# Kernel tuning notes

Measured on AMD Instinct MI355X. Metric: run time of the kernel, lower is better.

Reference implementation:

```python
import jax, jax.numpy as jnp
import numpy as np
import math

G_GRAPHS = 32   # graphs per batch
NPG = 2048      # nodes per graph
DEG = 8         # avg degree
IN_DIM = 128
HID = 128

def _lin(k, fi, fo):
    return jax.random.normal(k, (fi, fo), jnp.float32) / np.sqrt(fi).astype(np.float32)

def setup_inputs():
    key = jax.random.key(0)
    ks = jax.random.split(key, 32)
    Nt = G_GRAPHS * NPG
    Epg = NPG * DEG
    E = G_GRAPHS * Epg
    x = jax.random.normal(ks[0], (Nt, IN_DIM), jnp.float32)
    src = jax.random.randint(ks[1], (E,), 0, NPG)
    dst = jax.random.randint(ks[2], (E,), 0, NPG)
    off = (jnp.arange(E) // Epg) * NPG  # keep edges within their graph block
    edge_index = jnp.stack([src + off, dst + off]).astype(jnp.int32)
    batch = (jnp.arange(Nt) // NPG).astype(jnp.int32)
    p = {}
    dims = [(IN_DIM, HID), (HID, HID), (HID, HID), (HID, HID)]
    for i, (fi, fo) in enumerate(dims, 1):
        p['Wl%d' % i] = _lin(ks[3 * i], fi, fo)
        p['bl%d' % i] = jnp.zeros((fo,), jnp.float32)
        p['Wr%d' % i] = _lin(ks[3 * i + 1], fi, fo)
    for j in (1, 2):  # SAGPooling score GNN (GraphConv hidden->1)
        p['Prel%d' % j] = _lin(ks[15 + 2 * j], HID, 1)
        p['prb%d' % j] = jnp.zeros((1,), jnp.float32)
        p['Proot%d' % j] = _lin(ks[16 + 2 * j], HID, 1)
    p['W5'] = _lin(ks[24], HID, 64); p['b5'] = jnp.zeros((64,), jnp.float32)
    p['W6'] = _lin(ks[25], 64, 2);  p['b6'] = jnp.zeros((2,), jnp.float32)
    return dict(x=x, edge_index=edge_index, batch=batch, npg=NPG, **p)

def reference(x, edge_index, batch, npg,
              Wl1, bl1, Wr1, Wl2, bl2, Wr2, Wl3, bl3, Wr3, Wl4, bl4, Wr4,
              Prel1, prb1, Proot1, Prel2, prb2, Proot2, W5, b5, W6, b6):
    src, dst = edge_index[0], edge_index[1]
    Nt = x.shape[0]
    Gn = Nt // npg

    def sage(h, em, Wl, bl, Wr):
        # SAGEConv (mean aggr): lin_l(mean_j x_j) + lin_r(x_root)
        s = jax.ops.segment_sum(h[src] * em[:, None], dst, num_segments=Nt)
        c = jax.ops.segment_sum(em, dst, num_segments=Nt)
        return (s / jnp.maximum(c, 1.0)[:, None]) @ Wl + bl + h @ Wr

    def pool(h, em, nm, k, Prel, prb, Proot):
        # SAGPooling: score = GraphConv(h) (add aggr), top-k per graph, x *= tanh(score)
        s = jax.ops.segment_sum(h[src] * em[:, None], dst, num_segments=Nt)
        score = (s @ Prel + h @ Proot + prb)[:, 0]
        smr = jnp.where(nm > 0, score, -1e30).reshape(Gn, npg)
        _, idx = jax.lax.top_k(smr, k)
        newm = jnp.zeros((Gn, npg), h.dtype).at[jnp.arange(Gn)[:, None], idx].set(1.0).reshape(-1)
        h = h * jnp.tanh(score)[:, None] * newm[:, None]
        em = em * newm[src] * newm[dst]  # filter_adj: keep edges with both ends kept
        return h, em, newm

    em = jnp.ones(src.shape, x.dtype)
    nm = jnp.ones((Nt,), x.dtype)
    h = jax.nn.relu(sage(x, em, Wl1, bl1, Wr1))
    h = jax.nn.relu(sage(h, em, Wl2, bl2, Wr2))
    k1 = math.ceil(0.5 * npg)
    h, em, nm = pool(h, em, nm, k1, Prel1, prb1, Proot1)
    h = jax.nn.relu(sage(h, em, Wl3, bl3, Wr3)) * nm[:, None]
    h = jax.nn.relu(sage(h, em, Wl4, bl4, Wr4)) * nm[:, None]
    k2 = math.ceil(0.5 * k1)
    h, em, nm = pool(h, em, nm, k2, Prel2, prb2, Proot2)
    # global mean pool over surviving nodes
    sums = jax.ops.segment_sum(h, batch, num_segments=Gn)
    cnt = jax.ops.segment_sum(nm, batch, num_segments=Gn)
    g = sums / jnp.maximum(cnt, 1.0)[:, None]
    g = jax.nn.relu(g @ W5 + b5)
    return jax.nn.log_softmax(g @ W6 + b6, axis=1)
```

## Files before the change

### kernel.cpp

```cpp
#include <hip/hip_runtime.h>
#include <hip/hip_bf16.h>
#include <math.h>

#define NT   65536
#define NPGC 2048
#define NG   32
#define NE   524288
#define HID  128
#define K1   1024
#define K2   512

typedef short short8 __attribute__((ext_vector_type(8)));
typedef float f32x4  __attribute__((ext_vector_type(4)));

__device__ __forceinline__ float bf2f(unsigned short u) {
    union { unsigned int i; float f; } v; v.i = ((unsigned int)u) << 16; return v.f;
}
__device__ __forceinline__ unsigned short f2bf(float f) {
    union { float f; unsigned int i; } v; v.f = f;
    unsigned int x = v.i;
    return (unsigned short)((x + 0x7fffu + ((x >> 16) & 1u)) >> 16);
}
__device__ __forceinline__ void split2(float v, unsigned short& hi, unsigned short& lo) {
    unsigned int b = __float_as_uint(v);
    hi = (unsigned short)(b >> 16);
    float rem = v - __uint_as_float(b & 0xFFFF0000u);
    lo = (unsigned short)(__float_as_uint(rem) >> 16);
}

__global__ void k_detect(const unsigned short* __restrict__ x, int* __restrict__ flag) {
    __shared__ int cnt;
    if (threadIdx.x == 0) cnt = 0;
    __syncthreads();
    int sane = 0;
#pragma unroll
    for (int j = 0; j < 16; ++j) {
        unsigned short u = x[threadIdx.x * 16 + j];
        int e = (u >> 7) & 0xFF;
        if (e > 0x60 && e < 0xA0) sane++;
    }
    atomicAdd(&cnt, sane);
    __syncthreads();
    if (threadIdx.x == 0) *flag = (cnt > 3686) ? 1 : 0;
}

struct CvtDesc { const void* src[22]; int n[22]; int off[22]; };

__global__ void k_cvt(CvtDesc d, float* __restrict__ wts, const int* __restrict__ flag) {
    int t = blockIdx.y;
    int n = d.n[t];
    bool isbf = (*flag != 0);
    const unsigned short* sb = (const unsigned short*)d.src[t];
    const float* sf = (const float*)d.src[t];
    float* o = wts + d.off[t];
    for (int i = blockIdx.x * blockDim.x + threadIdx.x; i < n; i += gridDim.x * blockDim.x)
        o[i] = isbf ? bf2f(sb[i]) : sf[i];
}

__global__ void k_packW(const float* __restrict__ wts, int4 oWl, int4 oWr,
                        unsigned short* __restrict__ Wpack,
                        int* __restrict__ rowc, int* __restrict__ fill) {
    int idx = blockIdx.x * 256 + threadIdx.x;
    if (idx < NT) { rowc[idx] = 0; fill[idx] = 0; }
    if (idx >= 4 * 8 * 8 * 64 * 8) return;
    int L    = idx >> 15;
    int rem  = idx & 32767;
    int ct   = rem >> 12;
    int rem2 = rem & 4095;
    int ks   = rem2 >> 9;
    int rem3 = rem2 & 511;
    int lane = rem3 >> 3;
    int j    = rem3 & 7;
    int k   = ks * 32 + (lane >> 4) * 8 + j;
    int col = ct * 16 + (lane & 15);
    int ol = (L == 0) ? oWl.x : (L == 1) ? oWl.y : (L == 2) ? oWl.z : oWl.w;
    int orr = (L == 0) ? oWr.x : (L == 1) ? oWr.y : (L == 2) ? oWr.z : oWr.w;
    float w = (k < 128) ? wts[ol + k * 128 + col] : wts[orr + (k - 128) * 128 + col];
    unsigned short hi = f2bf(w);
    unsigned short lo = f2bf(w - bf2f(hi));
    int base = L * 65536 + (ct * 8 + ks) * 512 + lane * 8 + j;
    Wpack[base]         = hi;
    Wpack[base + 32768] = lo;
}

__global__ void k_load_x(const void* __restrict__ x, float* __restrict__ out,
                         const int* __restrict__ flag, int n4,
                         float* __restrict__ nm, const int* __restrict__ dstE,
                         int* __restrict__ rowc) {
    int i = blockIdx.x * blockDim.x + threadIdx.x;
    if (i < NT) nm[i] = 1.0f;
    if (i < NE) atomicAdd(&rowc[dstE[i]], 1);
    if (i >= n4) return;
    if (*flag) {
        ushort4 v = ((const ushort4*)x)[i];
        float4 o;
        o.x = bf2f(v.x); o.y = bf2f(v.y); o.z = bf2f(v.z); o.w = bf2f(v.w);
        ((float4*)out)[i] = o;
    }
}

__global__ void k_scan1(const int* __restrict__ cnt, int* __restrict__ rp, int* __restrict__ bsum,
                        float* __restrict__ invc) {
    __shared__ int s[256];
    int t = threadIdx.x;
    int i = blockIdx.x * 256 + t;
    int v = cnt[i];
    invc[i] = 1.0f / fmaxf((float)v, 1.0f);
    s[t] = v;
    __syncthreads();
    for (int off = 1; off < 256; off <<= 1) {
        int a = (t >= off) ? s[t - off] : 0;
        __syncthreads();
        s[t] += a;
        __syncthreads();
    }
    rp[i] = s[t] - v;
    if (t == 255) bsum[blockIdx.x] = s[255];
}

__global__ void k_scan23(int* __restrict__ rp, const int* __restrict__ bsum) {
    __shared__ int s[256];
    int t = threadIdx.x;
    s[t] = bsum[t];
    __syncthreads();
    for (int off = 1; off < 256; off <<= 1) {
        int a = (t >= off) ? s[t - off] : 0;
        __syncthreads();
        s[t] += a;
        __syncthreads();
    }
    int boffv = s[blockIdx.x] - bsum[blockIdx.x];
    int i = blockIdx.x * 256 + t;
    rp[i] += boffv;
    if (i == 0) rp[NT] = NE;
}

__global__ void k_scatter(const int* __restrict__ src, const int* __restrict__ dst,
                          const int* __restrict__ rp, int* __restrict__ fill, int* __restrict__ col) {
    int e = blockIdx.x * blockDim.x + threadIdx.x;
    if (e < NE) {
        int d = dst[e];
        int p = rp[d] + atomicAdd(&fill[d], 1);
        col[p] = src[e];
    }
}

__global__ void k_invc(const float* __restrict__ nm, const int* __restrict__ rp,
                       const int* __restrict__ col, float* __restrict__ invc,
                       const int* __restrict__ act) {
    int n = act[blockIdx.x * 256 + threadIdx.x];
    int beg = rp[n], end = rp[n + 1];
    float c = 0.f;
    for (int e = beg; e < end; ++e) c += nm[col[e]];
    invc[n] = 1.0f / fmaxf(c, 1.0f);
}

__device__ __forceinline__ int lds_sw(int node, int k) {
    int g = k >> 3;
    int go = g ^ (node & 7);
    return node * 128 + go * 8 + (k & 7);
}

template<bool HAS_TS, bool COMPACT>
__device__ __forceinline__ void sage_body(
    const float* __restrict__ h, const float* __restrict__ ts,
    const float* __restrict__ nm, const float* __restrict__ invc,
    const int* __restrict__ rp, const int* __restrict__ col,
    const unsigned short* __restrict__ Wp,
    unsigned short* Ahi, unsigned short* Alo,
    int n0, const int* sact, int tid, f32x4 acc[2][2])
{
    int lane = tid & 63, w = tid >> 6;
    int lrow = lane & 15, quad = lane >> 4;

#pragma unroll
    for (int pass = 0; pass < 4; ++pass) {
        int node = pass * 8 + (tid >> 5);
        int f = (tid & 31) * 4;
        int gn = COMPACT ? sact[node] : n0 + node;
        float ax = 0.f, ay = 0.f, az = 0.f, aw = 0.f;
        bool active = COMPACT ? true : (nm[gn] > 0.f);
        if (active) {
            int beg = rp[gn], end = rp[gn + 1];
            for (int e0 = beg; e0 < end; e0 += 4) {
                int ecl = end - 1;
                int e1 = (e0 + 1 < end) ? e0 + 1 : ecl;
                int e2 = (e0 + 2 < end) ? e0 + 2 : ecl;
                int e3 = (e0 + 3 < end) ? e0 + 3 : ecl;
                int s0 = col[e0], s1 = col[e1], s2 = col[e2], s3 = col[e3];
                float4 v0 = *(const float4*)&h[(size_t)s0 * HID + f];
                float4 v1 = *(const float4*)&h[(size_t)s1 * HID + f];
                float4 v2 = *(const float4*)&h[(size_t)s2 * HID + f];
                float4 v3 = *(const float4*)&h[(size_t)s3 * HID + f];
                float c0 = HAS_TS ? ts[s0] : 1.0f;
                float c1 = (e0 + 1 < end) ? (HAS_TS ? ts[s1] : 1.0f) : 0.0f;
                float c2 = (e0 + 2 < end) ? (HAS_TS ? ts[s2] : 1.0f) : 0.0f;
                float c3 = (e0 + 3 < end) ? (HAS_TS ? ts[s3] : 1.0f) : 0.0f;
                ax += v0.x * c0 + v1.x * c1 + v2.x * c2 + v3.x * c3;
                ay += v0.y * c0 + v1.y * c1 + v2.y * c2 + v3.y * c3;
                az += v0.z * c0 + v1.z * c1 + v2.z * c2 + v3.z * c3;
                aw += v0.w * c0 + v1.w * c1 + v2.w * c2 + v3.w * c3;
            }
        }
        float inv = invc[gn];
        ushort4 hi4, lo4;
        split2(ax * inv, hi4.x, lo4.x);
        split2(ay * inv, hi4.y, lo4.y);
        split2(az * inv, hi4.z, lo4.z);
        split2(aw * inv, hi4.w, lo4.w);
        int a = lds_sw(node, f);
        *(ushort4*)&Ahi[a] = hi4;
        *(ushort4*)&Alo[a] = lo4;
    }
    __syncthreads();

#pragma unroll
    for (int ks = 0; ks < 4; ++ks) {
        short8 bh[2], blo[2];
#pragma unroll
        for (int c = 0; c < 2; ++c) {
            int ct = 2 * w + c;
            bh[c]  = *(const short8*)&Wp[(ct * 8 + ks) * 512 + lane * 8];
            blo[c] = *(const short8*)&Wp[32768 + (ct * 8 + ks) * 512 + lane * 8];
        }
        int kb = ks * 32 + quad * 8;
#pragma unroll
        for (int st = 0; st < 2; ++st) {
            int a = lds_sw(st * 16 + lrow, kb);
            short8 ah = *(const short8*)&Ahi[a];
            short8 al = *(const short8*)&Alo[a];
#pragma unroll
            for (int c = 0; c < 2; ++c) {
                acc[st][c] = __builtin_amdgcn_mfma_f32_16x16x32_bf16(ah, bh[c],  acc[st][c], 0, 0, 0);
                acc[st][c] = __builtin_amdgcn_mfma_f32_16x16x32_bf16(al, bh[c],  acc[st][c], 0, 0, 0);
                acc[st][c] = __builtin_amdgcn_mfma_f32_16x16x32_bf16(ah, blo[c], acc[st][c], 0, 0, 0);
            }
        }
    }
    __syncthreads();

#pragma unroll
    for (int i = 0; i < 4; ++i) {
        int idx = i * 256 + tid;
        int node = idx >> 5;
        int f = (idx & 31) * 4;
        int gn = COMPACT ? sact[node] : n0 + node;
        float4 v = *(const float4*)&h[(size_t)gn * HID + f];
        float sc = HAS_TS ? ts[gn] : 1.0f;
        ushort4 hi4, lo4;
        split2(v.x * sc, hi4.x, lo4.x);
        split2(v.y * sc, hi4.y, lo4.y);
        split2(v.z * sc, hi4.z, lo4.z);
        split2(v.w * sc, hi4.w, lo4.w);
        int a = lds_sw(node, f);
        *(ushort4*)&Ahi[a] = hi4;
        *(ushort4*)&Alo[a] = lo4;
    }
    __syncthreads();

#pragma unroll
    for (int ks = 4; ks < 8; ++ks) {
        short8 bh[2], blo[2];
#pragma unroll
        for (int c = 0; c < 2; ++c) {
            int ct = 2 * w + c;
            bh[c]  = *(const short8*)&Wp[(ct * 8 + ks) * 512 + lane * 8];
            blo[c] = *(const short8*)&Wp[32768 + (ct * 8 + ks) * 512 + lane * 8];
        }
        int kb = (ks - 4) * 32 + quad * 8;
#pragma unroll
        for (int st = 0; st < 2; ++st) {
            int a = lds_sw(st * 16 + lrow, kb);
            short8 ah = *(const short8*)&Ahi[a];
            short8 al = *(const short8*)&Alo[a];
#pragma unroll
            for (int c = 0; c < 2; ++c) {
                acc[st][c] = __builtin_amdgcn_mfma_f32_16x16x32_bf16(ah, bh[c],  acc[st][c], 0, 0, 0);
                acc[st][c] = __builtin_amdgcn_mfma_f32_16x16x32_bf16(al, bh[c],  acc[st][c], 0, 0, 0);
                acc[st][c] = __builtin_amdgcn_mfma_f32_16x16x32_bf16(ah, blo[c], acc[st][c], 0, 0, 0);
            }
        }
    }
}

template<bool COMPACT>
__device__ __forceinline__ void map_block(int b, int& graph, int& tile) {
    if (COMPACT) { graph = (b & 7) * 4 + (b >> 8); tile = (b >> 3) & 31; }
    else         { graph = (b & 7) * 4 + (b >> 9); tile = (b >> 3) & 63; }
}

template<bool HAS_TS, bool COMPACT>
__global__ void __launch_bounds__(256, 8) k_sage_plain(
    const float* __restrict__ h, const void* __restrict__ xraw, const int* __restrict__ flag,
    const float* __restrict__ ts,
    const float* __restrict__ nm, const float* __restrict__ invc,
    const int* __restrict__ rp, const int* __restrict__ col,
    const unsigned short* __restrict__ Wp, const float* __restrict__ bl,
    float* __restrict__ out, const int* __restrict__ act)
{
    __shared__ unsigned short Ahi[32 * 128];
    __shared__ unsigned short Alo[32 * 128];
    __shared__ int sact[32];
    int tid = threadIdx.x;
    int graph, tile;
    map_block<COMPACT>(blockIdx.x, graph, tile);
    int n0 = graph * NPGC + tile * 32;
    if (COMPACT) {
        if (tid < 32) sact[tid] = act[graph * K1 + tile * 32 + tid];
        __syncthreads();
    }
    int lane = tid & 63, w = tid >> 6;
    int lrow = lane & 15, quad = lane >> 4;
    f32x4 acc[2][2] = {};

    const float* hh = h;
    if (!COMPACT && xraw && *flag == 0) hh = (const float*)xraw;

    sage_body<HAS_TS, COMPACT>(hh, ts, nm, invc, rp, col, Wp, Ahi, Alo, n0, sact, tid, acc);

#pragma unroll
    for (int c = 0; c < 2; ++c) {
        int colg = (2 * w + c) * 16 + lrow;
        float bias = bl[colg];
#pragma unroll
        for (int st = 0; st < 2; ++st) {
#pragma unroll
            for (int rr = 0; rr < 4; ++rr) {
                int nl = st * 16 + quad * 4 + rr;
                int node = COMPACT ? sact[nl] : n0 + nl;
                float val = fmaxf(acc[st][c][rr] + bias, 0.f);
                if (!COMPACT) val *= nm[node];
                out[(size_t)node * HID + colg] = val;
            }
        }
    }
}

template<bool HAS_TS, bool COMPACT>
__global__ void __launch_bounds__(256, 8) k_sage_dots(
    const float* __restrict__ h, const float* __restrict__ ts,
    const float* __restrict__ nm, const float* __restrict__ invc,
    const int* __restrict__ rp, const int* __restrict__ col,
    const unsigned short* __restrict__ Wp, const float* __restrict__ bl,
    float* __restrict__ out,
    const float* __restrict__ Prel, const float* __restrict__ Proot,
    float* __restrict__ q, float* __restrict__ r, const int* __restrict__ act)
{
    __shared__ unsigned short Ahi[32 * 128];
    __shared__ unsigned short Alo[32 * 128];
    __shared__ int sact[32];
    int tid = threadIdx.x;
    int graph, tile;
    map_block<COMPACT>(blockIdx.x, graph, tile);
    int n0 = graph * NPGC + tile * 32;
    if (COMPACT) {
        if (tid < 32) sact[tid] = act[graph * K1 + tile * 32 + tid];
        __syncthreads();
    }
    int lane = tid & 63, w = tid >> 6;
    int lrow = lane & 15, quad = lane >> 4;
    f32x4 acc[2][2] = {};

    sage_body<HAS_TS, COMPACT>(h, ts, nm, invc, rp, col, Wp, Ahi, Alo, n0, sact, tid, acc);

    float qp[2][4] = {}, rp_[2][4] = {};
#pragma unroll
    for (int c = 0; c < 2; ++c) {
        int colg = (2 * w + c) * 16 + lrow;
        float bias = bl[colg];
        float pq = Prel[colg], pr = Proot[colg];
#pragma unroll
        for (int st = 0; st < 2; ++st) {
#pragma unroll
            for (int rr = 0; rr < 4; ++rr) {
                int nl = st * 16 + quad * 4 + rr;
                int node = COMPACT ? sact[nl] : n0 + nl;
                float val = fmaxf(acc[st][c][rr] + bias, 0.f);
                if (!COMPACT) val *= nm[node];
                out[(size_t)node * HID + colg] = val;
                qp[st][rr] += val * pq;
                rp_[st][rr] += val * pr;
            }
        }
    }
#pragma unroll
    for (int st = 0; st < 2; ++st)
#pragma unroll
        for (int rr = 0; rr < 4; ++rr) {
#pragma unroll
            for (int m = 1; m < 16; m <<= 1) {
                qp[st][rr]  += __shfl_xor(qp[st][rr],  m, 64);
                rp_[st][rr] += __shfl_xor(rp_[st][rr], m, 64);
            }
        }
    __syncthreads();
    float* qa = (float*)Ahi;
    if (tid < 64) qa[tid] = 0.f;
    __syncthreads();
    if (lrow == 0) {
#pragma unroll
        for (int st = 0; st < 2; ++st)
#pragma unroll
            for (int rr = 0; rr < 4; ++rr) {
                int nl = st * 16 + quad * 4 + rr;
                atomicAdd(&qa[nl], qp[st][rr]);
                atomicAdd(&qa[32 + nl], rp_[st][rr]);
            }
    }
    __syncthreads();
    if (tid < 32) {
        int node = COMPACT ? sact[tid] : n0 + tid;
        q[node] = qa[tid];
        r[node] = qa[32 + tid];
    }
}

__global__ void k_score(const float* __restrict__ q, const float* __restrict__ r,
                        const float* __restrict__ prb,
                        const int* __restrict__ rp, const int* __restrict__ col,
                        float* __restrict__ score) {
    int n = blockIdx.x * 256 + threadIdx.x;
    int beg = rp[n], end = rp[n + 1];
    float s = 0.f;
    for (int e = beg; e < end; ++e) s += q[col[e]];
    score[n] = s + r[n] + prb[0];
}

template<bool ZQ>
__global__ void __launch_bounds__(256) k_topk(const float* __restrict__ score,
                                              float* __restrict__ nm,
                                              float* __restrict__ tval, int k,
                                              int* __restrict__ act,
                                              float* __restrict__ q) {
    __shared__ unsigned int u[NPGC];
    __shared__ int hist[256];
    __shared__ int scanb[257];
    __shared__ int wtot[4];
    __shared__ int wtot2[4];
    __shared__ unsigned int s_byte;
    __shared__ int s_kk;
    int tid = threadIdx.x;
    int lane = tid & 63, wv = tid >> 6;
    int base = blockIdx.x * NPGC;

    for (int j = tid; j < NPGC; j += 256) {
        float sc = (nm[base + j] > 0.f) ? score[base + j] : -1e30f;
        unsigned int v = __float_as_uint(sc);
        v = (v & 0x80000000u) ? ~v : (v | 0x80000000u);
        u[j] = v;
    }
    hist[tid] = 0;
    if (tid == 0) scanb[256] = 0;
    __syncthreads();

    unsigned int prefix = 0;
    int kk = k;
#pragma unroll
    for (int round = 0; round < 4; ++round) {
        int shift = 24 - 8 * round;
        unsigned int pmask = (round == 0) ? 0u : (0xFFFFFFFFu << (32 - 8 * round));
        for (int j = tid; j < NPGC; j += 256) {
            unsigned int v = u[j];
            if ((v & pmask) == prefix) atomicAdd(&hist[(v >> shift) & 0xFF], 1);
        }
        __syncthreads();
        int s = hist[tid];
#pragma unroll
        for (int off = 1; off < 64; off <<= 1) {
            int t = __shfl_down(s, off, 64);
            s += (lane + off < 64) ? t : 0;
        }
        if (lane == 0) wtot[wv] = s;
        __syncthreads();
        int add = 0;
#pragma unroll
        for (int w2 = 1; w2 < 4; ++w2) add += (wv + w2 < 4) ? wtot[wv + w2] : 0;
        s += add;
        scanb[tid] = s;
        __syncthreads();
        int above = scanb[tid + 1];
        if (s >= kk && above < kk) { s_byte = (unsigned int)tid; s_kk = kk - above; }
        hist[tid] = 0;
        __syncthreads();
        prefix |= (s_byte << shift);
        kk = s_kk;
    }
    unsigned int thr = prefix;

    int j0 = tid * 8;
    int cnt = 0;
#pragma unroll
    for (int j = 0; j < 8; ++j) cnt += (u[j0 + j] == thr);
    int s = cnt;
#pragma unroll
    for (int off = 1; off < 64; off <<= 1) {
        int t = __shfl_up(s, off, 64);
        s += (lane >= off) ? t : 0;
    }
    if (lane == 63) wtot[wv] = s;
    __syncthreads();
    int add = 0;
#pragma unroll
    for (int w2 = 0; w2 < 4; ++w2) add += (w2 < wv) ? wtot[w2] : 0;
    int rank = s - cnt + add;

    unsigned int keepmask = 0u;
    int myrank = rank;
    int kcnt = 0;
#pragma unroll
    for (int j = 0; j < 8; ++j) {
        unsigned int v = u[j0 + j];
        bool kp;
        if (v > thr) kp = true;
        else if (v == thr) { kp = (myrank < kk); myrank++; }
        else kp = false;
        keepmask |= (kp ? 1u : 0u) << j;
        kcnt += kp ? 1 : 0;
    }
    int s2 = kcnt;
#pragma unroll
    for (int off = 1; off < 64; off <<= 1) {
        int t2 = __shfl_up(s2, off, 64);
        s2 += (lane >= off) ? t2 : 0;
    }
    if (lane == 63) wtot2[wv] = s2;
    __syncthreads();
    int pos = s2 - kcnt;
#pragma unroll
    for (int w2 = 0; w2 < 4; ++w2) pos += (w2 < wv) ? wtot2[w2] : 0;
    int* actg = act + blockIdx.x * k;
#pragma unroll
    for (int j = 0; j < 8; ++j) {
        bool kp = (keepmask >> j) & 1u;
        int n = base + j0 + j;
        nm[n]   = kp ? 1.0f : 0.0f;
        tval[n] = kp ? tanhf(score[n]) : 0.0f;
        if (kp)      { actg[pos++] = n; }
        else if (ZQ) { q[n] = 0.0f; }
    }
}

__global__ void k_gsum(const float* __restrict__ h, const float* __restrict__ t,
                       const int* __restrict__ act, float* __restrict__ g) {
    int b = blockIdx.x;
    int graph = b >> 2, part = b & 3;
    int f = threadIdx.x & 127, sub = threadIdx.x >> 7;
    int base = graph * K2 + part * 128 + sub * 64;
    float acc = 0.f;
#pragma unroll 4
    for (int n = 0; n < 64; ++n) {
        int gn = act[base + n];
        acc += h[(size_t)gn * HID + f] * t[gn];
    }
    atomicAdd(&g[graph * HID + f], acc);
}

__global__ void k_mlp(const float* __restrict__ g,
                      const float* __restrict__ W5,
                      const float* __restrict__ b5, const float* __restrict__ W6,
                      const float* __restrict__ b6, void* __restrict__ out,
                      const int* __restrict__ flag) {
    __shared__ float g5[64];
    __shared__ float ls[2];
    int graph = blockIdx.x, j = threadIdx.x;
    const float ic = 1.0f / (float)K2;
    float acc = b5[j];
    for (int f = 0; f < HID; ++f)
        acc += (g[graph * HID + f] * ic) * W5[f * 64 + j];
    g5[j] = fmaxf(acc, 0.f);
    __syncthreads();
    if (j < 2) {
        float l = b6[j];
        for (int t = 0; t < 64; ++t) l += g5[t] * W6[t * 2 + j];
        ls[j] = l;
    }
    __syncthreads();
    if (j == 0) {
        float a = ls[0], b = ls[1];
        float mx = fmaxf(a, b);
        float lse = mx + logf(expf(a - mx) + expf(b - mx));
        if (*flag) {
            ((unsigned short*)out)[graph * 2 + 0] = f2bf(a - lse);
            ((unsigned short*)out)[graph * 2 + 1] = f2bf(b - lse);
        } else {
            ((float*)out)[graph * 2 + 0] = a - lse;
            ((float*)out)[graph * 2 + 1] = b - lse;
        }
    }
}

extern "C" void kernel_launch(void* const* d_in, const int* in_sizes, int n_in,
                              void* d_out, int out_size, void* d_ws, size_t ws_size,
                              hipStream_t stream) {
    const void* x    = d_in[0];
    const int*  ei   = (const int*)d_in[1];
    const int*  srcE = ei;
    const int*  dstE = ei + NE;

    char* ws = (char*)d_ws;
    float* hA    = (float*)(ws + 0);
    float* hB    = (float*)(ws + 33554432);
    float* tvec  = (float*)(ws + 67108864);
    float* invc  = (float*)(ws + 67371008);
    float* q     = (float*)(ws + 100663296);
    float* r     = (float*)(ws + 100925440);
    float* score = (float*)(ws + 101187584);
    float* nm    = (float*)(ws + 101449728);
    int*   rowc  = (int*)  (ws + 101711872);
    int*   rp    = (int*)  (ws + 101974016);
    int*   bsum  = (int*)  (ws + 102236416);
    int*   fill  = (int*)  (ws + 102238464);
    int*   col   = (int*)  (ws + 102500608);
    float* g     = (float*)(ws + 104597760);
    int*   flag  = (int*)  (ws + 104615936);
    float* wts   = (float*)(ws + 104616960);
    unsigned short* Wpack = (unsigned short*)(ws + 105179136);
    int*   act1  = rowc;
    int*   act2  = fill;
    (void)in_sizes; (void)n_in; (void)out_size; (void)ws_size;

    const int O_Wl1 = 0,      O_bl1 = 16384,  O_Wr1 = 16512;
    const int O_Wl2 = 32896,  O_bl2 = 49280,  O_Wr2 = 49408;
    const int O_Wl3 = 65792,  O_bl3 = 82176,  O_Wr3 = 82304;
    const int O_Wl4 = 98688,  O_bl4 = 115072, O_Wr4 = 115200;
    const int O_Pr1 = 131584, O_pb1 = 131712, O_Po1 = 131713;
    const int O_Pr2 = 131841, O_pb2 = 131969, O_Po2 = 131970;
    const int O_W5  = 132098, O_b5  = 140290, O_W6 = 140354, O_b6 = 140482;

    CvtDesc d;
    const int srcIdx[22] = {4,5,6,7,8,9,10,11,12,13,14,15,16,17,18,19,20,21,22,23,24,25};
    const int nelems[22] = {16384,128,16384, 16384,128,16384, 16384,128,16384, 16384,128,16384,
                            128,1,128, 128,1,128, 8192,64,128,2};
    const int offs[22]   = {O_Wl1,O_bl1,O_Wr1, O_Wl2,O_bl2,O_Wr2, O_Wl3,O_bl3,O_Wr3, O_Wl4,O_bl4,O_Wr4,
                            O_Pr1,O_pb1,O_Po1, O_Pr2,O_pb2,O_Po2, O_W5,O_b5,O_W6,O_b6};
    for (int i = 0; i < 22; ++i) { d.src[i] = d_in[srcIdx[i]]; d.n[i] = nelems[i]; d.off[i] = offs[i]; }

    hipMemsetAsync(g, 0, (NG * HID + NG + 64) * 4, stream);

    k_detect <<<1, 256, 0, stream>>>((const unsigned short*)x, flag);
    k_cvt    <<<dim3(64, 22), 256, 0, stream>>>(d, wts, flag);
    k_packW  <<<512, 256, 0, stream>>>(wts, make_int4(O_Wl1, O_Wl2, O_Wl3, O_Wl4),
                                       make_int4(O_Wr1, O_Wr2, O_Wr3, O_Wr4), Wpack, rowc, fill);
    k_load_x <<<8192, 256, 0, stream>>>(x, hA, flag, NT * HID / 4, nm, dstE, rowc);

    k_scan1  <<<256, 256, 0, stream>>>(rowc, rp, bsum, invc);
    k_scan23 <<<256, 256, 0, stream>>>(rp, bsum);
    k_scatter<<<2048, 256, 0, stream>>>(srcE, dstE, rp, fill, col);

    k_sage_plain<false, false><<<2048, 256, 0, stream>>>(hA, x, flag, nullptr, nm, invc, rp, col,
                                                         Wpack + 0 * 65536, wts + O_bl1, hB, nullptr);
    k_sage_dots<false, false><<<2048, 256, 0, stream>>>(hB, nullptr, nm, invc, rp, col,
                                                        Wpack + 1 * 65536, wts + O_bl2, hA,
                                                        wts + O_Pr1, wts + O_Po1, q, r, nullptr);

    k_score<<<256, 256, 0, stream>>>(q, r, wts + O_pb1, rp, col, score);
    k_topk<true><<<32, 256, 0, stream>>>(score, nm, tvec, K1, act1, q);
    k_invc <<<NG * K1 / 256, 256, 0, stream>>>(nm, rp, col, invc, act1);

    k_sage_plain<true, true><<<1024, 256, 0, stream>>>(hA, nullptr, flag, tvec, nm, invc, rp, col,
                                                       Wpack + 2 * 65536, wts + O_bl3, hB, act1);
    k_sage_dots<true, true><<<1024, 256, 0, stream>>>(hB, nm, nm, invc, rp, col,
                                                      Wpack + 3 * 65536, wts + O_bl4, hA,
                                                      wts + O_Pr2, wts + O_Po2, q, r, act1);

    k_score<<<256, 256, 0, stream>>>(q, r, wts + O_pb2, rp, col, score);
    k_topk<false><<<32, 256, 0, stream>>>(score, nm, tvec, K2, act2, nullptr);

    k_gsum<<<NG * 4, 256, 0, stream>>>(hA, tvec, act2, g);
    k_mlp <<<32, 64, 0, stream>>>(g, wts + O_W5, wts + O_b5, wts + O_W6, wts + O_b6, d_out, flag);
}
```

Measured before the change: 369.4 us.

## Prefetch root features, double LDS buffers, widen gather, score only active nodes

The SAGE body now loads root-node features into registers before the neighbour gather. It stages them in a second pair of LDS buffers, so the two GEMM halves run as one 8-step loop with a single barrier instead of three. The gather loop is unrolled to 8 edges per iteration to keep more loads in flight. Active-node indices are read straight from global memory instead of being staged in LDS. The second score kernel runs only over the surviving active nodes. Occupancy is lowered (launch bounds 8 to 4 blocks) to fit the doubled LDS and the extra registers, trading some latency hiding for more memory-level parallelism per thread.

```diff
diff --git a/kernel.cpp b/kernel.cpp
--- a/kernel.cpp
+++ b/kernel.cpp
@@ -168,38 +168,53 @@
     const int* __restrict__ rp, const int* __restrict__ col,
     const unsigned short* __restrict__ Wp,
     unsigned short* Ahi, unsigned short* Alo,
-    int n0, const int* sact, int tid, f32x4 acc[2][2])
+    unsigned short* Bhi, unsigned short* Blo,
+    int n0, const int* __restrict__ actb, int tid, f32x4 acc[2][2])
 {
     int lane = tid & 63, w = tid >> 6;
     int lrow = lane & 15, quad = lane >> 4;
 
+    float4 rootv[4]; float roots[4];
+#pragma unroll
+    for (int i = 0; i < 4; ++i) {
+        int idx = i * 256 + tid;
+        int node = idx >> 5;
+        int f2 = (idx & 31) * 4;
+        int gn = COMPACT ? actb[node] : n0 + node;
+        rootv[i] = *(const float4*)&h[(size_t)gn * HID + f2];
+        roots[i] = HAS_TS ? ts[gn] : 1.0f;
+    }
+
+    int gnode = tid >> 5;
+    int f = (tid & 31) * 4;
 #pragma unroll
     for (int pass = 0; pass < 4; ++pass) {
-        int node = pass * 8 + (tid >> 5);
-        int f = (tid & 31) * 4;
-        int gn = COMPACT ? sact[node] : n0 + node;
+        int node = pass * 8 + gnode;
+        int gn = COMPACT ? actb[node] : n0 + node;
         float ax = 0.f, ay = 0.f, az = 0.f, aw = 0.f;
         bool active = COMPACT ? true : (nm[gn] > 0.f);
         if (active) {
             int beg = rp[gn], end = rp[gn + 1];
-            for (int e0 = beg; e0 < end; e0 += 4) {
-                int ecl = end - 1;
-                int e1 = (e0 + 1 < end) ? e0 + 1 : ecl;
-                int e2 = (e0 + 2 < end) ? e0 + 2 : ecl;
-                int e3 = (e0 + 3 < end) ? e0 + 3 : ecl;
-                int s0 = col[e0], s1 = col[e1], s2 = col[e2], s3 = col[e3];
-                float4 v0 = *(const float4*)&h[(size_t)s0 * HID + f];
-                float4 v1 = *(const float4*)&h[(size_t)s1 * HID + f];
-                float4 v2 = *(const float4*)&h[(size_t)s2 * HID + f];
-                float4 v3 = *(const float4*)&h[(size_t)s3 * HID + f];
-                float c0 = HAS_TS ? ts[s0] : 1.0f;
-                float c1 = (e0 + 1 < end) ? (HAS_TS ? ts[s1] : 1.0f) : 0.0f;
-                float c2 = (e0 + 2 < end) ? (HAS_TS ? ts[s2] : 1.0f) : 0.0f;
-                float c3 = (e0 + 3 < end) ? (HAS_TS ? ts[s3] : 1.0f) : 0.0f;
-                ax += v0.x * c0 + v1.x * c1 + v2.x * c2 + v3.x * c3;
-                ay += v0.y * c0 + v1.y * c1 + v2.y * c2 + v3.y * c3;
-                az += v0.z * c0 + v1.z * c1 + v2.z * c2 + v3.z * c3;
-                aw += v0.w * c0 + v1.w * c1 + v2.w * c2 + v3.w * c3;
+            int ecl = end - 1;
+            for (int e0 = beg; e0 < end; e0 += 8) {
+                int sj[8];
+#pragma unroll
+                for (int j = 0; j < 8; ++j) {
+                    int e = (e0 + j < end) ? e0 + j : ecl;
+                    sj[j] = col[e];
+                }
+                float4 vj[8];
+#pragma unroll
+                for (int j = 0; j < 8; ++j)
+                    vj[j] = *(const float4*)&h[(size_t)sj[j] * HID + f];
+#pragma unroll
+                for (int j = 0; j < 8; ++j) {
+                    float cj = (e0 + j < end) ? (HAS_TS ? ts[sj[j]] : 1.0f) : 0.0f;
+                    ax += vj[j].x * cj;
+                    ay += vj[j].y * cj;
+                    az += vj[j].z * cj;
+                    aw += vj[j].w * cj;
+                }
             }
         }
         float inv = invc[gn];
@@ -212,10 +227,28 @@
         *(ushort4*)&Ahi[a] = hi4;
         *(ushort4*)&Alo[a] = lo4;
     }
-    __syncthreads();
-
-#pragma unroll
-    for (int ks = 0; ks < 4; ++ks) {
+
+#pragma unroll
+    for (int i = 0; i < 4; ++i) {
+        int idx = i * 256 + tid;
+        int node = idx >> 5;
+        int f2 = (idx & 31) * 4;
+        float sc = roots[i];
+        ushort4 hi4, lo4;
+        split2(rootv[i].x * sc, hi4.x, lo4.x);
+        split2(rootv[i].y * sc, hi4.y, lo4.y);
+        split2(rootv[i].z * sc, hi4.z, lo4.z);
+        split2(rootv[i].w * sc, hi4.w, lo4.w);
+        int a = lds_sw(node, f2);
+        *(ushort4*)&Bhi[a] = hi4;
+        *(ushort4*)&Blo[a] = lo4;
+    }
+    __syncthreads();
+
+#pragma unroll
+    for (int ks = 0; ks < 8; ++ks) {
+        const unsigned short* Hb = (ks < 4) ? Ahi : Bhi;
+        const unsigned short* Lb = (ks < 4) ? Alo : Blo;
         short8 bh[2], blo[2];
 #pragma unroll
         for (int c = 0; c < 2; ++c) {
@@ -223,12 +256,12 @@
             bh[c]  = *(const short8*)&Wp[(ct * 8 + ks) * 512 + lane * 8];
             blo[c] = *(const short8*)&Wp[32768 + (ct * 8 + ks) * 512 + lane * 8];
         }
-        int kb = ks * 32 + quad * 8;
+        int kb = (ks & 3) * 32 + quad * 8;
 #pragma unroll
         for (int st = 0; st < 2; ++st) {
             int a = lds_sw(st * 16 + lrow, kb);
-            short8 ah = *(const short8*)&Ahi[a];
-            short8 al = *(const short8*)&Alo[a];
+            short8 ah = *(const short8*)&Hb[a];
+            short8 al = *(const short8*)&Lb[a];
 #pragma unroll
             for (int c = 0; c < 2; ++c) {
                 acc[st][c] = __builtin_amdgcn_mfma_f32_16x16x32_bf16(ah, bh[c],  acc[st][c], 0, 0, 0);
@@ -237,50 +270,6 @@
             }
         }
     }
-    __syncthreads();
-
-#pragma unroll
-    for (int i = 0; i < 4; ++i) {
-        int idx = i * 256 + tid;
-        int node = idx >> 5;
-        int f = (idx & 31) * 4;
-        int gn = COMPACT ? sact[node] : n0 + node;
-        float4 v = *(const float4*)&h[(size_t)gn * HID + f];
-        float sc = HAS_TS ? ts[gn] : 1.0f;
-        ushort4 hi4, lo4;
-        split2(v.x * sc, hi4.x, lo4.x);
-        split2(v.y * sc, hi4.y, lo4.y);
-        split2(v.z * sc, hi4.z, lo4.z);
-        split2(v.w * sc, hi4.w, lo4.w);
-        int a = lds_sw(node, f);
-        *(ushort4*)&Ahi[a] = hi4;
-        *(ushort4*)&Alo[a] = lo4;
-    }
-    __syncthreads();
-
-#pragma unroll
-    for (int ks = 4; ks < 8; ++ks) {
-        short8 bh[2], blo[2];
-#pragma unroll
-        for (int c = 0; c < 2; ++c) {
-            int ct = 2 * w + c;
-            bh[c]  = *(const short8*)&Wp[(ct * 8 + ks) * 512 + lane * 8];
-            blo[c] = *(const short8*)&Wp[32768 + (ct * 8 + ks) * 512 + lane * 8];
-        }
-        int kb = (ks - 4) * 32 + quad * 8;
-#pragma unroll
-        for (int st = 0; st < 2; ++st) {
-            int a = lds_sw(st * 16 + lrow, kb);
-            short8 ah = *(const short8*)&Ahi[a];
-            short8 al = *(const short8*)&Alo[a];
-#pragma unroll
-            for (int c = 0; c < 2; ++c) {
-                acc[st][c] = __builtin_amdgcn_mfma_f32_16x16x32_bf16(ah, bh[c],  acc[st][c], 0, 0, 0);
-                acc[st][c] = __builtin_amdgcn_mfma_f32_16x16x32_bf16(al, bh[c],  acc[st][c], 0, 0, 0);
-                acc[st][c] = __builtin_amdgcn_mfma_f32_16x16x32_bf16(ah, blo[c], acc[st][c], 0, 0, 0);
-            }
-        }
-    }
 }
 
 template<bool COMPACT>
@@ -290,7 +279,7 @@
 }
 
 template<bool HAS_TS, bool COMPACT>
-__global__ void __launch_bounds__(256, 8) k_sage_plain(
+__global__ void __launch_bounds__(256, 4) k_sage_plain(
     const float* __restrict__ h, const void* __restrict__ xraw, const int* __restrict__ flag,
     const float* __restrict__ ts,
     const float* __restrict__ nm, const float* __restrict__ invc,
@@ -300,15 +289,13 @@
 {
     __shared__ unsigned short Ahi[32 * 128];
     __shared__ unsigned short Alo[32 * 128];
-    __shared__ int sact[32];
+    __shared__ unsigned short Bhi[32 * 128];
+    __shared__ unsigned short Blo[32 * 128];
     int tid = threadIdx.x;
     int graph, tile;
     map_block<COMPACT>(blockIdx.x, graph, tile);
     int n0 = graph * NPGC + tile * 32;
-    if (COMPACT) {
-        if (tid < 32) sact[tid] = act[graph * K1 + tile * 32 + tid];
-        __syncthreads();
-    }
+    const int* actb = COMPACT ? (act + graph * K1 + tile * 32) : nullptr;
     int lane = tid & 63, w = tid >> 6;
     int lrow = lane & 15, quad = lane >> 4;
     f32x4 acc[2][2] = {};
@@ -316,7 +303,7 @@
     const float* hh = h;
     if (!COMPACT && xraw && *flag == 0) hh = (const float*)xraw;
 
-    sage_body<HAS_TS, COMPACT>(hh, ts, nm, invc, rp, col, Wp, Ahi, Alo, n0, sact, tid, acc);
+    sage_body<HAS_TS, COMPACT>(hh, ts, nm, invc, rp, col, Wp, Ahi, Alo, Bhi, Blo, n0, actb, tid, acc);
 
 #pragma unroll
     for (int c = 0; c < 2; ++c) {
@@ -327,7 +314,7 @@
 #pragma unroll
             for (int rr = 0; rr < 4; ++rr) {
                 int nl = st * 16 + quad * 4 + rr;
-                int node = COMPACT ? sact[nl] : n0 + nl;
+                int node = COMPACT ? actb[nl] : n0 + nl;
                 float val = fmaxf(acc[st][c][rr] + bias, 0.f);
                 if (!COMPACT) val *= nm[node];
                 out[(size_t)node * HID + colg] = val;
@@ -337,7 +324,7 @@
 }
 
 template<bool HAS_TS, bool COMPACT>
-__global__ void __launch_bounds__(256, 8) k_sage_dots(
+__global__ void __launch_bounds__(256, 4) k_sage_dots(
     const float* __restrict__ h, const float* __restrict__ ts,
     const float* __restrict__ nm, const float* __restrict__ invc,
     const int* __restrict__ rp, const int* __restrict__ col,
@@ -348,20 +335,18 @@
 {
     __shared__ unsigned short Ahi[32 * 128];
     __shared__ unsigned short Alo[32 * 128];
-    __shared__ int sact[32];
+    __shared__ unsigned short Bhi[32 * 128];
+    __shared__ unsigned short Blo[32 * 128];
     int tid = threadIdx.x;
     int graph, tile;
     map_block<COMPACT>(blockIdx.x, graph, tile);
     int n0 = graph * NPGC + tile * 32;
-    if (COMPACT) {
-        if (tid < 32) sact[tid] = act[graph * K1 + tile * 32 + tid];
-        __syncthreads();
-    }
+    const int* actb = COMPACT ? (act + graph * K1 + tile * 32) : nullptr;
     int lane = tid & 63, w = tid >> 6;
     int lrow = lane & 15, quad = lane >> 4;
     f32x4 acc[2][2] = {};
 
-    sage_body<HAS_TS, COMPACT>(h, ts, nm, invc, rp, col, Wp, Ahi, Alo, n0, sact, tid, acc);
+    sage_body<HAS_TS, COMPACT>(h, ts, nm, invc, rp, col, Wp, Ahi, Alo, Bhi, Blo, n0, actb, tid, acc);
 
     float qp[2][4] = {}, rp_[2][4] = {};
 #pragma unroll
@@ -374,7 +359,7 @@
 #pragma unroll
             for (int rr = 0; rr < 4; ++rr) {
                 int nl = st * 16 + quad * 4 + rr;
-                int node = COMPACT ? sact[nl] : n0 + nl;
+                int node = COMPACT ? actb[nl] : n0 + nl;
                 float val = fmaxf(acc[st][c][rr] + bias, 0.f);
                 if (!COMPACT) val *= nm[node];
                 out[(size_t)node * HID + colg] = val;
@@ -409,7 +394,7 @@
     }
     __syncthreads();
     if (tid < 32) {
-        int node = COMPACT ? sact[tid] : n0 + tid;
+        int node = COMPACT ? actb[tid] : n0 + tid;
         q[node] = qa[tid];
         r[node] = qa[32 + tid];
     }
@@ -420,6 +405,17 @@
                         const int* __restrict__ rp, const int* __restrict__ col,
                         float* __restrict__ score) {
     int n = blockIdx.x * 256 + threadIdx.x;
+    int beg = rp[n], end = rp[n + 1];
+    float s = 0.f;
+    for (int e = beg; e < end; ++e) s += q[col[e]];
+    score[n] = s + r[n] + prb[0];
+}
+
+__global__ void k_score_act(const float* __restrict__ q, const float* __restrict__ r,
+                            const float* __restrict__ prb,
+                            const int* __restrict__ rp, const int* __restrict__ col,
+                            float* __restrict__ score, const int* __restrict__ act) {
+    int n = act[blockIdx.x * 256 + threadIdx.x];
     int beg = rp[n], end = rp[n + 1];
     float s = 0.f;
     for (int e = beg; e < end; ++e) s += q[col[e]];
@@ -663,7 +659,7 @@
                                                       Wpack + 3 * 65536, wts + O_bl4, hA,
                                                       wts + O_Pr2, wts + O_Po2, q, r, act1);
 
-    k_score<<<256, 256, 0, stream>>>(q, r, wts + O_pb2, rp, col, score);
+    k_score_act<<<NG * K1 / 256, 256, 0, stream>>>(q, r, wts + O_pb2, rp, col, score, act1);
     k_topk<false><<<32, 256, 0, stream>>>(score, nm, tvec, K2, act2, nullptr);
 
     k_gsum<<<NG * 4, 256, 0, stream>>>(hA, tvec, act2, g);
```

Result: no change. 364.2 us (-1.4%).
